# Kernel tuning notes

Measured on AMD Instinct MI355X. Metric: run time of the kernel, lower is better.

## Reference

```python
import jax, jax.numpy as jnp
import numpy as np

B, S, D, H = 2, 2048, 1024, 16
DH = D // H


def setup_inputs() -> dict:
    key = jax.random.key(0)
    ks = jax.random.split(key, 11)
    s = 0.02
    return {
        "queries": jax.random.normal(ks[0], (B, S, D), dtype=jnp.float32),
        "keys": jax.random.normal(ks[1], (B, S, D), dtype=jnp.float32),
        "values": jax.random.normal(ks[2], (B, S, D), dtype=jnp.float32),
        "Wq": jax.random.normal(ks[3], (D, D), dtype=jnp.float32) * s,
        "bq": jnp.zeros((D,), dtype=jnp.float32),
        "Wk": jax.random.normal(ks[4], (D, D), dtype=jnp.float32) * s,
        "bk": jnp.zeros((D,), dtype=jnp.float32),
        "Wv": jax.random.normal(ks[5], (D, D), dtype=jnp.float32) * s,
        "bv": jnp.zeros((D,), dtype=jnp.float32),
        "Wo": jax.random.normal(ks[6], (D, D), dtype=jnp.float32) * s,
        "bo": jnp.zeros((D,), dtype=jnp.float32),
    }


def _split_heads(x):
    # [B,S,D] -> [B,H,S,Dh]
    b, s, _ = x.shape
    return x.reshape(b, s, H, DH).transpose(0, 2, 1, 3)


def reference(queries, keys, values, Wq, bq, Wk, bk, Wv, bv, Wo, bo):
    q = _split_heads(queries @ Wq + bq)   # [B,H,S,Dh]
    k = _split_heads(keys @ Wk + bk)
    v = _split_heads(values @ Wv + bv)
    # d_k in the original is the last dim AFTER head split -> head_dim
    scale = 1.0 / jnp.sqrt(jnp.float32(DH))
    scores = jnp.einsum("bhqd,bhkd->bhqk", q, k) * scale  # [B,H,S,S]
    weights = jax.nn.softmax(scores, axis=-1)
    o = jnp.einsum("bhqk,bhkd->bhqd", weights, v)         # [B,H,S,Dh]
    o = o.transpose(0, 2, 1, 3).reshape(queries.shape[0], queries.shape[1], D)
    return o @ Wo + bo
```

## Files before the change

### kernel.cpp

```cpp
#include <hip/hip_runtime.h>
#include <stdint.h>

#define B_ 2
#define S_ 2048
#define D_ 1024
#define H_ 16
#define DH_ 64
#define M_ 4096

typedef unsigned short u16;
typedef unsigned int u32;
typedef short mfma_elem_t;
typedef mfma_elem_t bfrag8 __attribute__((ext_vector_type(8)));
typedef float floatx4 __attribute__((ext_vector_type(4)));

__device__ __forceinline__ u16 f2bf(float f) {
  unsigned u = __float_as_uint(f);
  u += 0x7fff + ((u >> 16) & 1);
  return (u16)(u >> 16);
}

__device__ __forceinline__ u32 pack_bf16(float a, float b) {
  u32 ua = __float_as_uint(a) + 0x8000u;
  u32 ub = __float_as_uint(b) + 0x8000u;
#if __has_builtin(__builtin_amdgcn_perm)
  return __builtin_amdgcn_perm(ub, ua, 0x07060302u);
#else
  return (ua >> 16) | (ub & 0xffff0000u);
#endif
}

__device__ __forceinline__ void gl_lds16(const void* g, void* l) {
  __builtin_amdgcn_global_load_lds(
      (__attribute__((address_space(1))) void*)(g),
      (__attribute__((address_space(3))) void*)(l), 16, 0, 0);
}

__global__ __launch_bounds__(256) void k_convert_x(
    const float* __restrict__ q, const float* __restrict__ k, const float* __restrict__ v,
    u16* __restrict__ xq, u16* __restrict__ xk, u16* __restrict__ xv) {
  const float* src = blockIdx.z == 0 ? q : (blockIdx.z == 1 ? k : v);
  u16* dst = blockIdx.z == 0 ? xq : (blockIdx.z == 1 ? xk : xv);
  int i = (blockIdx.x * 256 + threadIdx.x) * 4;
  float4 f = *(const float4*)(src + i);
  ushort4 o;
  o.x = f2bf(f.x); o.y = f2bf(f.y); o.z = f2bf(f.z); o.w = f2bf(f.w);
  *(ushort4*)(dst + i) = o;
}

__global__ __launch_bounds__(256) void k_convert_w(
    const float* __restrict__ wq, const float* __restrict__ wk,
    const float* __restrict__ wv, const float* __restrict__ wo,
    u16* __restrict__ tq, u16* __restrict__ tk, u16* __restrict__ tv, u16* __restrict__ to_) {
  const int gz = blockIdx.z;
  const float* w = gz == 0 ? wq : gz == 1 ? wk : gz == 2 ? wv : wo;
  u16* t = gz == 0 ? tq : gz == 1 ? tk : gz == 2 ? tv : to_;
  __shared__ float tile[32][33];
  int r0 = blockIdx.y * 32, c0 = blockIdx.x * 32;
  int tx = threadIdx.x, ty = threadIdx.y;
#pragma unroll
  for (int i = 0; i < 4; i++) {
    int r = ty + i * 8;
    tile[r][tx] = w[(size_t)(r0 + r) * D_ + c0 + tx];
  }
  __syncthreads();
#pragma unroll
  for (int i = 0; i < 4; i++) {
    int r = ty + i * 8;
    t[(size_t)(c0 + r) * D_ + r0 + tx] = f2bf(tile[tx][r]);
  }
}

__global__ __launch_bounds__(256, 3) void k_gemm_qkv(
    const u16* __restrict__ xq, const u16* __restrict__ xk, const u16* __restrict__ xv,
    const u16* __restrict__ wtq, const u16* __restrict__ wtk, const u16* __restrict__ wtv,
    const float* __restrict__ bq, const float* __restrict__ bk, const float* __restrict__ bv,
    u16* __restrict__ oq, u16* __restrict__ ok, u16* __restrict__ ovt) {
  const int gz = blockIdx.z;
  const u16* X = gz == 0 ? xq : gz == 1 ? xk : xv;
  const u16* WT = gz == 0 ? wtq : gz == 1 ? wtk : wtv;
  const float* bias = gz == 0 ? bq : gz == 1 ? bk : bv;
  u16* outsd = gz == 0 ? oq : ok;
  const float qscale = gz == 0 ? 0.125f * 1.4426950408889634f : 1.0f;

  __shared__ u16 sbuf[2][8192];

  const int t = threadIdx.x;
  const int w = t >> 6, lane = t & 63, l15 = lane & 15, quad = lane >> 4;
  const int wm = (w >> 1) * 64, wn = (w & 1) * 64;
  const int m0 = blockIdx.y * 128, n0 = blockIdx.x * 128;

  floatx4 acc[4][4];
  floatx4 zero = {0.f, 0.f, 0.f, 0.f};
#pragma unroll
  for (int mt = 0; mt < 4; mt++)
#pragma unroll
    for (int nt = 0; nt < 4; nt++) acc[mt][nt] = zero;

  auto stage = [&](int kt, int b) {
    int k0 = kt * 32;
#pragma unroll
    for (int i = 0; i < 2; i++) {
      int chunk = i * 256 + t;
      gl_lds16(X + (size_t)(m0 + (chunk >> 2)) * D_ + k0 + (chunk & 3) * 8,
               sbuf[b] + i * 2048 + w * 512);
      gl_lds16(WT + (size_t)(n0 + (chunk >> 2)) * D_ + k0 + (chunk & 3) * 8,
               sbuf[b] + 4096 + i * 2048 + w * 512);
    }
  };

  stage(0, 0);
  for (int kt = 0; kt < 32; kt++) {
    __syncthreads();
    if (kt < 31) stage(kt + 1, (kt + 1) & 1);
    const u16* As = sbuf[kt & 1];
    const u16* Bs = sbuf[kt & 1] + 4096;
    bfrag8 af[4], bf[4];
#pragma unroll
    for (int mt = 0; mt < 4; mt++)
      af[mt] = *(const bfrag8*)(As + (wm + mt * 16 + l15) * 32 + quad * 8);
#pragma unroll
    for (int nt = 0; nt < 4; nt++)
      bf[nt] = *(const bfrag8*)(Bs + (wn + nt * 16 + l15) * 32 + quad * 8);
#pragma unroll
    for (int mt = 0; mt < 4; mt++)
#pragma unroll
      for (int nt = 0; nt < 4; nt++)
        acc[mt][nt] = __builtin_amdgcn_mfma_f32_16x16x32_bf16(af[mt], bf[nt], acc[mt][nt], 0, 0, 0);
  }

  if (gz < 2) {
#pragma unroll
    for (int mt = 0; mt < 4; mt++)
#pragma unroll
      for (int nt = 0; nt < 4; nt++) {
        int Nc = n0 + wn + nt * 16 + l15;
        float bv_ = bias[Nc];
        int hh = Nc >> 6, dh = Nc & 63;
#pragma unroll
        for (int r = 0; r < 4; r++) {
          int Mr = m0 + wm + mt * 16 + quad * 4 + r;
          int bb = Mr >> 11, ss = Mr & 2047;
          outsd[((size_t)(bb * H_ + hh) * S_ + ss) * DH_ + dh] =
              f2bf((acc[mt][nt][r] + bv_) * qscale);
        }
      }
  } else {
#pragma unroll
    for (int mt = 0; mt < 4; mt++)
#pragma unroll
      for (int nt = 0; nt < 4; nt++) {
        int Nc = n0 + wn + nt * 16 + l15;
        float bv_ = bias[Nc];
        int hh = Nc >> 6, dh = Nc & 63;
        int Mr0 = m0 + wm + mt * 16 + quad * 4;
        int bb = Mr0 >> 11, ss0 = Mr0 & 2047;
        ushort4 o;
        o.x = f2bf(acc[mt][nt][0] + bv_);
        o.y = f2bf(acc[mt][nt][1] + bv_);
        o.z = f2bf(acc[mt][nt][2] + bv_);
        o.w = f2bf(acc[mt][nt][3] + bv_);
        *(ushort4*)(ovt + ((size_t)(bb * H_ + hh) * DH_ + dh) * S_ + ss0) = o;
      }
  }
}

__global__ __launch_bounds__(256, 3) void k_gemm_final(
    const u16* __restrict__ X, const u16* __restrict__ WT,
    const float* __restrict__ bias, float* __restrict__ out) {
  __shared__ u16 sbuf[2][8192];
  const int t = threadIdx.x;
  const int w = t >> 6, lane = t & 63, l15 = lane & 15, quad = lane >> 4;
  const int wm = (w >> 1) * 64, wn = (w & 1) * 64;
  const int m0 = blockIdx.y * 128, n0 = blockIdx.x * 128;

  floatx4 acc[4][4];
  floatx4 zero = {0.f, 0.f, 0.f, 0.f};
#pragma unroll
  for (int mt = 0; mt < 4; mt++)
#pragma unroll
    for (int nt = 0; nt < 4; nt++) acc[mt][nt] = zero;

  auto stage = [&](int kt, int b) {
    int k0 = kt * 32;
#pragma unroll
    for (int i = 0; i < 2; i++) {
      int chunk = i * 256 + t;
      gl_lds16(X + (size_t)(m0 + (chunk >> 2)) * D_ + k0 + (chunk & 3) * 8,
               sbuf[b] + i * 2048 + w * 512);
      gl_lds16(WT + (size_t)(n0 + (chunk >> 2)) * D_ + k0 + (chunk & 3) * 8,
               sbuf[b] + 4096 + i * 2048 + w * 512);
    }
  };

  stage(0, 0);
  for (int kt = 0; kt < 32; kt++) {
    __syncthreads();
    if (kt < 31) stage(kt + 1, (kt + 1) & 1);
    const u16* As = sbuf[kt & 1];
    const u16* Bs = sbuf[kt & 1] + 4096;
    bfrag8 af[4], bf[4];
#pragma unroll
    for (int mt = 0; mt < 4; mt++)
      af[mt] = *(const bfrag8*)(As + (wm + mt * 16 + l15) * 32 + quad * 8);
#pragma unroll
    for (int nt = 0; nt < 4; nt++)
      bf[nt] = *(const bfrag8*)(Bs + (wn + nt * 16 + l15) * 32 + quad * 8);
#pragma unroll
    for (int mt = 0; mt < 4; mt++)
#pragma unroll
      for (int nt = 0; nt < 4; nt++)
        acc[mt][nt] = __builtin_amdgcn_mfma_f32_16x16x32_bf16(af[mt], bf[nt], acc[mt][nt], 0, 0, 0);
  }
#pragma unroll
  for (int mt = 0; mt < 4; mt++)
#pragma unroll
    for (int nt = 0; nt < 4; nt++) {
      int Nc = n0 + wn + nt * 16 + l15;
      float bv_ = bias[Nc];
#pragma unroll
      for (int r = 0; r < 4; r++) {
        int Mr = m0 + wm + mt * 16 + quad * 4 + r;
        out[(size_t)Mr * D_ + Nc] = acc[mt][nt][r] + bv_;
      }
    }
}

__global__ __launch_bounds__(256, 2) void k_attn(
    const u16* __restrict__ Q, const u16* __restrict__ K,
    const u16* __restrict__ Vt, u16* __restrict__ O) {
  __shared__ u16 lds[25600];

  const int t = threadIdx.x, w = t >> 6, lane = t & 63, l15 = lane & 15, quad = lane >> 4;
  const int bh = blockIdx.z * H_ + blockIdx.y;
  const int q0 = blockIdx.x * 128;
  const int qh = (w >> 1) * 64;
  const int kh = (w & 1) * 64;
  const u16* Qb = Q + (size_t)bh * S_ * DH_;
  const u16* Kb = K + (size_t)bh * S_ * DH_;
  const u16* Vb = Vt + (size_t)bh * DH_ * S_;
  u16* Pw = lds + 16384 + w * 2304;

  bfrag8 qf[4][2];
#pragma unroll
  for (int qt = 0; qt < 4; qt++)
#pragma unroll
    for (int ks = 0; ks < 2; ks++)
      qf[qt][ks] = *(const bfrag8*)(Qb + (size_t)(q0 + qh + qt * 16 + l15) * DH_ + ks * 32 + quad * 8);

  floatx4 oacc[4][4];
  float lrow[4] = {0.f, 0.f, 0.f, 0.f};
  floatx4 zero = {0.f, 0.f, 0.f, 0.f};
#pragma unroll
  for (int qt = 0; qt < 4; qt++)
#pragma unroll
    for (int dt = 0; dt < 4; dt++) oacc[qt][dt] = zero;

  for (int kt = 0; kt < 16; kt++) {
    const int kv0 = kt * 128;
#pragma unroll
    for (int i = 0; i < 4; i++) {
      int chunk = i * 256 + t;
      gl_lds16(Kb + (size_t)(kv0 + ((chunk >> 2) & 127)) * DH_ + (chunk >> 9) * 32 + (chunk & 3) * 8,
               lds + i * 2048 + w * 512);
      gl_lds16(Vb + (size_t)(t >> 2) * S_ + kv0 + i * 32 + (t & 3) * 8,
               lds + 8192 + i * 2048 + w * 512);
    }
    __syncthreads();

    floatx4 sacc[4][4];
#pragma unroll
    for (int nt = 0; nt < 4; nt++) {
      bfrag8 kf0 = *(const bfrag8*)(lds + (kh + nt * 16 + l15) * 32 + quad * 8);
      bfrag8 kf1 = *(const bfrag8*)(lds + 4096 + (kh + nt * 16 + l15) * 32 + quad * 8);
#pragma unroll
      for (int qt = 0; qt < 4; qt++) {
        floatx4 s0 = __builtin_amdgcn_mfma_f32_16x16x32_bf16(kf0, qf[qt][0], zero, 0, 0, 0);
        sacc[nt][qt] = __builtin_amdgcn_mfma_f32_16x16x32_bf16(kf1, qf[qt][1], s0, 0, 0, 0);
      }
    }

#pragma unroll
    for (int c = 0; c < 2; c++) {
#pragma unroll
      for (int j = 0; j < 2; j++) {
        const int nt = c * 2 + j;
#pragma unroll
        for (int qt = 0; qt < 4; qt++) {
          float p0 = __builtin_amdgcn_exp2f(sacc[nt][qt][0]);
          float p1 = __builtin_amdgcn_exp2f(sacc[nt][qt][1]);
          float p2 = __builtin_amdgcn_exp2f(sacc[nt][qt][2]);
          float p3 = __builtin_amdgcn_exp2f(sacc[nt][qt][3]);
          lrow[qt] += (p0 + p1) + (p2 + p3);
          uint2 pd;
          pd.x = pack_bf16(p0, p1);
          pd.y = pack_bf16(p2, p3);
          *(uint2*)(Pw + (qt * 16 + l15) * 36 + j * 16 + quad * 4) = pd;
        }
      }
      bfrag8 pf[4];
#pragma unroll
      for (int qt = 0; qt < 4; qt++)
        pf[qt] = *(const bfrag8*)(Pw + (qt * 16 + l15) * 36 + quad * 8);
#pragma unroll
      for (int dt = 0; dt < 4; dt++) {
        bfrag8 vf = *(const bfrag8*)(lds + 8192 + ((w & 1) * 2 + c) * 2048 + (dt * 16 + l15) * 32 + quad * 8);
#pragma unroll
        for (int qt = 0; qt < 4; qt++)
          oacc[qt][dt] = __builtin_amdgcn_mfma_f32_16x16x32_bf16(vf, pf[qt], oacc[qt][dt], 0, 0, 0);
      }
    }
    __syncthreads();
  }

  float* ocmb = (float*)lds;
  float* lcmb = (float*)lds + 8704;
  const int p = w >> 1;

#pragma unroll
  for (int qt = 0; qt < 4; qt++) {
    float l = lrow[qt];
    l += __shfl_xor(l, 16, 64);
    l += __shfl_xor(l, 32, 64);
    lrow[qt] = l;
  }

  if (w & 1) {
    float* po = ocmb + p * 4352;
#pragma unroll
    for (int qt = 0; qt < 4; qt++) {
#pragma unroll
      for (int dt = 0; dt < 4; dt++)
        *(floatx4*)(po + (qt * 16 + l15) * 68 + dt * 16 + quad * 4) = oacc[qt][dt];
      if (quad == 0) lcmb[p * 64 + qt * 16 + l15] = lrow[qt];
    }
  }
  __syncthreads();
  if (!(w & 1)) {
    float* po = ocmb + p * 4352;
#pragma unroll
    for (int qt = 0; qt < 4; qt++) {
      float rinv = 1.0f / (lrow[qt] + lcmb[p * 64 + qt * 16 + l15]);
      int qrow = q0 + qh + qt * 16 + l15;
#pragma unroll
      for (int dt = 0; dt < 4; dt++) {
        floatx4 oo = oacc[qt][dt] + *(const floatx4*)(po + (qt * 16 + l15) * 68 + dt * 16 + quad * 4);
        ushort4 o;
        o.x = f2bf(oo[0] * rinv);
        o.y = f2bf(oo[1] * rinv);
        o.z = f2bf(oo[2] * rinv);
        o.w = f2bf(oo[3] * rinv);
        *(ushort4*)(O + ((size_t)blockIdx.z * S_ + qrow) * D_ + blockIdx.y * DH_ + dt * 16 + quad * 4) = o;
      }
    }
  }
}

extern "C" void kernel_launch(void* const* d_in, const int* in_sizes, int n_in,
                              void* d_out, int out_size, void* d_ws, size_t ws_size,
                              hipStream_t stream) {
  const float* queries = (const float*)d_in[0];
  const float* keys = (const float*)d_in[1];
  const float* values = (const float*)d_in[2];
  const float* Wq = (const float*)d_in[3];
  const float* bq = (const float*)d_in[4];
  const float* Wk = (const float*)d_in[5];
  const float* bk = (const float*)d_in[6];
  const float* Wv = (const float*)d_in[7];
  const float* bv = (const float*)d_in[8];
  const float* Wo = (const float*)d_in[9];
  const float* bo = (const float*)d_in[10];

  const size_t NXB = (size_t)M_ * D_ * 2;
  const size_t WB = (size_t)D_ * D_ * 2;
  if (ws_size < 7 * NXB + 4 * WB) return;

  char* ws = (char*)d_ws;
  u16* Xq = (u16*)(ws);
  u16* Xk = (u16*)(ws + NXB);
  u16* Xv = (u16*)(ws + 2 * NXB);
  u16* WqT = (u16*)(ws + 3 * NXB);
  u16* WkT = (u16*)(ws + 3 * NXB + WB);
  u16* WvT = (u16*)(ws + 3 * NXB + 2 * WB);
  u16* WoT = (u16*)(ws + 3 * NXB + 3 * WB);
  char* ws2 = ws + 3 * NXB + 4 * WB;
  u16* Qhs = (u16*)(ws2);
  u16* Khs = (u16*)(ws2 + NXB);
  u16* VtB = (u16*)(ws2 + 2 * NXB);
  u16* Obuf = (u16*)(ws2 + 3 * NXB);
  float* outp = (float*)d_out;

  k_convert_x<<<dim3(4096, 1, 3), 256, 0, stream>>>(queries, keys, values, Xq, Xk, Xv);
  k_convert_w<<<dim3(32, 32, 4), dim3(32, 8), 0, stream>>>(Wq, Wk, Wv, Wo, WqT, WkT, WvT, WoT);
  k_gemm_qkv<<<dim3(8, 32, 3), 256, 0, stream>>>(Xq, Xk, Xv, WqT, WkT, WvT, bq, bk, bv, Qhs, Khs, VtB);
  k_attn<<<dim3(16, 16, 2), 256, 0, stream>>>(Qhs, Khs, VtB, Obuf);
  k_gemm_final<<<dim3(8, 32), 256, 0, stream>>>(Obuf, WoT, bo, outp);
}
```

Baseline: 238.4 us.

## Double-buffer K/V tiles in attention kernel with smaller 64-key steps

The attention loop changes from 16 iterations over 128-key tiles with load-then-sync to 32 iterations over 64-key tiles. K and V for the next tile are prefetched into a second LDS buffer while the current tile is computed. This removes one barrier per iteration and lets global-to-LDS loads overlap with MFMA work. In exchange, each iteration does less compute per barrier, and the loop runs twice as many times with smaller per-wave S/P tiles.

```diff
diff --git a/kernel.cpp b/kernel.cpp
--- a/kernel.cpp
+++ b/kernel.cpp
@@ -235,7 +235,7 @@
   const int bh = blockIdx.z * H_ + blockIdx.y;
   const int q0 = blockIdx.x * 128;
   const int qh = (w >> 1) * 64;
-  const int kh = (w & 1) * 64;
+  const int kvh = w & 1;
   const u16* Qb = Q + (size_t)bh * S_ * DH_;
   const u16* Kb = K + (size_t)bh * S_ * DH_;
   const u16* Vb = Vt + (size_t)bh * DH_ * S_;
@@ -248,6 +248,19 @@
     for (int ks = 0; ks < 2; ks++)
       qf[qt][ks] = *(const bfrag8*)(Qb + (size_t)(q0 + qh + qt * 16 + l15) * DH_ + ks * 32 + quad * 8);
 
+  auto stage = [&](int kv0, int b) {
+    u16* Kbuf = lds + b * 8192;
+    u16* Vbuf = lds + b * 8192 + 4096;
+#pragma unroll
+    for (int ks = 0; ks < 2; ks++)
+      gl_lds16(Kb + (size_t)(kv0 + (t >> 2)) * DH_ + ks * 32 + (t & 3) * 8,
+               Kbuf + ks * 2048 + w * 512);
+#pragma unroll
+    for (int ksp = 0; ksp < 2; ksp++)
+      gl_lds16(Vb + (size_t)(t >> 2) * S_ + kv0 + ksp * 32 + (t & 3) * 8,
+               Vbuf + ksp * 2048 + w * 512);
+  };
+
   floatx4 oacc[4][4];
   float lrow[4] = {0.f, 0.f, 0.f, 0.f};
   floatx4 zero = {0.f, 0.f, 0.f, 0.f};
@@ -256,23 +269,18 @@
 #pragma unroll
     for (int dt = 0; dt < 4; dt++) oacc[qt][dt] = zero;
 
-  for (int kt = 0; kt < 16; kt++) {
-    const int kv0 = kt * 128;
-#pragma unroll
-    for (int i = 0; i < 4; i++) {
-      int chunk = i * 256 + t;
-      gl_lds16(Kb + (size_t)(kv0 + ((chunk >> 2) & 127)) * DH_ + (chunk >> 9) * 32 + (chunk & 3) * 8,
-               lds + i * 2048 + w * 512);
-      gl_lds16(Vb + (size_t)(t >> 2) * S_ + kv0 + i * 32 + (t & 3) * 8,
-               lds + 8192 + i * 2048 + w * 512);
-    }
+  stage(0, 0);
+  for (int kt = 0; kt < 32; kt++) {
     __syncthreads();
-
-    floatx4 sacc[4][4];
-#pragma unroll
-    for (int nt = 0; nt < 4; nt++) {
-      bfrag8 kf0 = *(const bfrag8*)(lds + (kh + nt * 16 + l15) * 32 + quad * 8);
-      bfrag8 kf1 = *(const bfrag8*)(lds + 4096 + (kh + nt * 16 + l15) * 32 + quad * 8);
+    if (kt < 31) stage((kt + 1) * 64, (kt + 1) & 1);
+    const u16* Kbuf = lds + (kt & 1) * 8192;
+    const u16* Vbuf = lds + (kt & 1) * 8192 + 4096;
+
+    floatx4 sacc[2][4];
+#pragma unroll
+    for (int nt = 0; nt < 2; nt++) {
+      bfrag8 kf0 = *(const bfrag8*)(Kbuf + (kvh * 32 + nt * 16 + l15) * 32 + quad * 8);
+      bfrag8 kf1 = *(const bfrag8*)(Kbuf + 2048 + (kvh * 32 + nt * 16 + l15) * 32 + quad * 8);
 #pragma unroll
       for (int qt = 0; qt < 4; qt++) {
         floatx4 s0 = __builtin_amdgcn_mfma_f32_16x16x32_bf16(kf0, qf[qt][0], zero, 0, 0, 0);
@@ -281,38 +289,34 @@
     }
 
 #pragma unroll
-    for (int c = 0; c < 2; c++) {
-#pragma unroll
-      for (int j = 0; j < 2; j++) {
-        const int nt = c * 2 + j;
-#pragma unroll
-        for (int qt = 0; qt < 4; qt++) {
-          float p0 = __builtin_amdgcn_exp2f(sacc[nt][qt][0]);
-          float p1 = __builtin_amdgcn_exp2f(sacc[nt][qt][1]);
-          float p2 = __builtin_amdgcn_exp2f(sacc[nt][qt][2]);
-          float p3 = __builtin_amdgcn_exp2f(sacc[nt][qt][3]);
-          lrow[qt] += (p0 + p1) + (p2 + p3);
-          uint2 pd;
-          pd.x = pack_bf16(p0, p1);
-          pd.y = pack_bf16(p2, p3);
-          *(uint2*)(Pw + (qt * 16 + l15) * 36 + j * 16 + quad * 4) = pd;
-        }
-      }
-      bfrag8 pf[4];
+    for (int nt = 0; nt < 2; nt++)
+#pragma unroll
+      for (int qt = 0; qt < 4; qt++) {
+        float p0 = __builtin_amdgcn_exp2f(sacc[nt][qt][0]);
+        float p1 = __builtin_amdgcn_exp2f(sacc[nt][qt][1]);
+        float p2 = __builtin_amdgcn_exp2f(sacc[nt][qt][2]);
+        float p3 = __builtin_amdgcn_exp2f(sacc[nt][qt][3]);
+        lrow[qt] += (p0 + p1) + (p2 + p3);
+        uint2 pd;
+        pd.x = pack_bf16(p0, p1);
+        pd.y = pack_bf16(p2, p3);
+        *(uint2*)(Pw + (qt * 16 + l15) * 36 + nt * 16 + quad * 4) = pd;
+      }
+
+    bfrag8 pf[4];
+#pragma unroll
+    for (int qt = 0; qt < 4; qt++)
+      pf[qt] = *(const bfrag8*)(Pw + (qt * 16 + l15) * 36 + quad * 8);
+#pragma unroll
+    for (int dt = 0; dt < 4; dt++) {
+      bfrag8 vf = *(const bfrag8*)(Vbuf + kvh * 2048 + (dt * 16 + l15) * 32 + quad * 8);
 #pragma unroll
       for (int qt = 0; qt < 4; qt++)
-        pf[qt] = *(const bfrag8*)(Pw + (qt * 16 + l15) * 36 + quad * 8);
-#pragma unroll
-      for (int dt = 0; dt < 4; dt++) {
-        bfrag8 vf = *(const bfrag8*)(lds + 8192 + ((w & 1) * 2 + c) * 2048 + (dt * 16 + l15) * 32 + quad * 8);
-#pragma unroll
-        for (int qt = 0; qt < 4; qt++)
-          oacc[qt][dt] = __builtin_amdgcn_mfma_f32_16x16x32_bf16(vf, pf[qt], oacc[qt][dt], 0, 0, 0);
-      }
-    }
-    __syncthreads();
-  }
-
+        oacc[qt][dt] = __builtin_amdgcn_mfma_f32_16x16x32_bf16(vf, pf[qt], oacc[qt][dt], 0, 0, 0);
+    }
+  }
+
+  __syncthreads();
   float* ocmb = (float*)lds;
   float* lcmb = (float*)lds + 8704;
   const int p = w >> 1;
```

Result: slower. 247.0 us (+3.6%).
